# Optimization experiments

Hardware: AMD Instinct MI355X
Metric: run time of the kernel (lower is better)

The kernel has to match this reference:

```python
import jax, jax.numpy as jnp
import numpy as np

B, N_PER = 8, 16
N_ROIS = B * N_PER
C_SLOW, T_SLOW = 1024, 8
C_FAST, T_FAST = 256, 32
HF, WF = 16, 16
C_CAT = 2048          # channels after slow/fast concat
C_OUT = 1024          # 2048 // temporal_pool_size
T_POOL = 2
C_FEAT = C_OUT * T_POOL  # 2048 channels of the rearranged 2D feature map
OUT_SIZE = 16         # RoIAlign output size
RATIO = 2             # sampling_ratio
SCALE = 1.0 / 16.0    # 1 / featmap_stride
GN_GROUPS = 16
EPS = 1e-5


def setup_inputs() -> dict:
    key = jax.random.key(0)
    ks = jax.random.split(key, 8)
    slow_feat = jax.random.normal(ks[0], (B, C_SLOW, T_SLOW, HF, WF), jnp.float32)
    fast_feat = jax.random.normal(ks[1], (B, C_FAST, T_FAST, HF, WF), jnp.float32)
    pos = jax.random.normal(ks[2], (1, C_FEAT, HF, WF), jnp.float32)
    conv_w = jax.random.normal(ks[3], (C_OUT, C_CAT), jnp.float32) / np.float32(np.sqrt(C_CAT))
    gn_gamma = jnp.ones((C_OUT,), jnp.float32)
    gn_beta = jnp.zeros((C_OUT,), jnp.float32)
    # rois: [N,5] = (batch_idx, x1, y1, x2, y2) in input-image coords (256px clip).
    # Equal count per clip and sorted by batch idx -> grouping is a static reshape.
    bidx = jnp.repeat(jnp.arange(B), N_PER).astype(jnp.float32)
    cx = jax.random.uniform(ks[4], (N_ROIS,), minval=32.0, maxval=224.0)
    cy = jax.random.uniform(ks[5], (N_ROIS,), minval=32.0, maxval=224.0)
    w = jax.random.uniform(ks[6], (N_ROIS,), minval=32.0, maxval=160.0)
    h = jax.random.uniform(ks[7], (N_ROIS,), minval=32.0, maxval=160.0)
    x1 = jnp.clip(cx - w / 2, 0.0, 255.0)
    x2 = jnp.clip(cx + w / 2, 0.0, 255.0)
    y1 = jnp.clip(cy - h / 2, 0.0, 255.0)
    y2 = jnp.clip(cy + h / 2, 0.0, 255.0)
    rois = jnp.stack([bidx, x1, y1, x2, y2], axis=1)
    return dict(slow_feat=slow_feat, fast_feat=fast_feat, rois=rois, pos=pos,
                conv_w=conv_w, gn_gamma=gn_gamma, gn_beta=gn_beta)


def trans_feat(slow_feat, fast_feat, conv_w, gn_gamma, gn_beta):
    Bb, Cf, Tf, Wf_, Hf_ = fast_feat.shape
    ratio = 32 // slow_feat.shape[2]  # int(32 / T_slow)
    # fast: [B,C,T,W,H] -> [B,W,H,T,C] -> [B,W,H,T//r, C*r] -> [B, C*r, T//r, W, H]
    f = jnp.transpose(fast_feat, (0, 3, 4, 2, 1)).reshape(Bb, Wf_, Hf_, Tf // ratio, Cf * ratio)
    f = jnp.transpose(f, (0, 4, 3, 1, 2))
    feat = jnp.concatenate([slow_feat, f], axis=1)  # [B, 2048, T_slow, W, H]
    Bc, Cc, Tc, Wc, Hc = feat.shape
    # AdaptiveAvgPool3d((T_POOL, None, None)), Tc divisible by T_POOL
    feat = feat.reshape(Bc, Cc, T_POOL, Tc // T_POOL, Wc, Hc).mean(axis=3)
    # 1x1x1 Conv3d (no bias) -> GroupNorm(16) -> ReLU
    y = jnp.einsum('oc,bcthw->bothw', conv_w, feat)
    yg = y.reshape(Bc, GN_GROUPS, C_OUT // GN_GROUPS, T_POOL, Wc, Hc)
    mu = yg.mean(axis=(2, 3, 4, 5), keepdims=True)
    var = ((yg - mu) ** 2).mean(axis=(2, 3, 4, 5), keepdims=True)
    yg = (yg - mu) * jax.lax.rsqrt(var + EPS)
    y = yg.reshape(Bc, C_OUT, T_POOL, Wc, Hc)
    y = y * gn_gamma[None, :, None, None, None] + gn_beta[None, :, None, None, None]
    y = jax.nn.relu(y)
    # rearrange 'b c t w h -> b (c t) w h'
    return y.reshape(Bc, C_OUT * T_POOL, Wc, Hc)


def roialign_weights(rois):
    # mmcv RoIAlign (aligned=True, avg pool, sampling_ratio=RATIO) as a sparse
    # linear map over flattened feature pixels: out[n,:,p] = Wmat[n,p,:] @ feat[n,:,:]
    x1 = rois[:, 1] * SCALE - 0.5
    y1 = rois[:, 2] * SCALE - 0.5
    x2 = rois[:, 3] * SCALE - 0.5
    y2 = rois[:, 4] * SCALE - 0.5
    bw = (x2 - x1) / OUT_SIZE
    bh = (y2 - y1) / OUT_SIZE
    grid = (jnp.arange(OUT_SIZE, dtype=jnp.float32)[:, None]
            + (jnp.arange(RATIO, dtype=jnp.float32)[None, :] + 0.5) / RATIO)  # [O, r]
    ys = y1[:, None, None] + grid[None] * bh[:, None, None]  # [N, O, r]
    xs = x1[:, None, None] + grid[None] * bw[:, None, None]
    Y = jnp.broadcast_to(ys[:, :, None, :, None], (N_ROIS, OUT_SIZE, OUT_SIZE, RATIO, RATIO))
    X = jnp.broadcast_to(xs[:, None, :, None, :], (N_ROIS, OUT_SIZE, OUT_SIZE, RATIO, RATIO))
    valid = ((Y >= -1.0) & (Y <= HF) & (X >= -1.0) & (X <= WF)).astype(jnp.float32)
    y = jnp.maximum(Y, 0.0)
    x = jnp.maximum(X, 0.0)
    y0f = jnp.floor(y)
    x0f = jnp.floor(x)
    ye = y0f >= HF - 1
    xe = x0f >= WF - 1
    y0 = jnp.where(ye, HF - 1, y0f).astype(jnp.int32)
    y1i = jnp.where(ye, HF - 1, y0f + 1).astype(jnp.int32)
    x0 = jnp.where(xe, WF - 1, x0f).astype(jnp.int32)
    x1i = jnp.where(xe, WF - 1, x0f + 1).astype(jnp.int32)
    ly = jnp.where(ye, 0.0, y - y0f)
    lx = jnp.where(xe, 0.0, x - x0f)
    hy = 1.0 - ly
    hx = 1.0 - lx
    cnt = float(RATIO * RATIO)
    w = jnp.stack([hy * hx, hy * lx, ly * hx, ly * lx], axis=-1) * (valid / cnt)[..., None]
    idx = jnp.stack([y0 * WF + x0, y0 * WF + x1i, y1i * WF + x0, y1i * WF + x1i], axis=-1)
    P = OUT_SIZE * OUT_SIZE
    K = RATIO * RATIO * 4
    idx = idx.reshape(N_ROIS, P, K)
    w = w.reshape(N_ROIS, P, K)
    Wmat = jnp.zeros((N_ROIS, P, HF * WF), jnp.float32)
    Wmat = Wmat.at[jnp.arange(N_ROIS)[:, None, None],
                   jnp.arange(P)[None, :, None], idx].add(w)
    return Wmat


def reference(slow_feat, fast_feat, rois, pos, conv_w, gn_gamma, gn_beta):
    feat = trans_feat(slow_feat, fast_feat, conv_w, gn_gamma, gn_beta)  # [B, 2048, 16, 16]
    Wmat = roialign_weights(rois)                 # [N, 256, 256]
    bidx = rois[:, 0].astype(jnp.int32)
    featN = feat[bidx].reshape(N_ROIS, C_FEAT, HF * WF)  # per-roi feature gather
    # RoIAlign -> AdaptiveAvgPool2d((1,1)) -> view(1, C)
    roi_feat = jnp.einsum('npq,ncq->ncp', Wmat, featN).mean(axis=-1)  # [N, 2048]
    posF = pos.reshape(C_FEAT, HF * WF)           # pos.repeat(B,...) is identical per clip
    roi_pos = jnp.einsum('npq,cq->ncp', Wmat, posF).mean(axis=-1)     # [N, 2048]
    # bucketing by batch idx; rois are sorted with N_PER per clip -> static reshape
    roi_feat_grouped = roi_feat.reshape(B, N_PER, C_FEAT)
    roi_pos_grouped = roi_pos.reshape(B, N_PER, C_FEAT)
    return feat, roi_feat_grouped, roi_pos_grouped
```

## Files before the change

kernel.cpp:

```cpp
#include <hip/hip_runtime.h>
#include <hip/hip_bf16.h>

#define WH 256
#define FEATSZ 4194304
#define ROISZ  262144

typedef short s16x4 __attribute__((ext_vector_type(4)));
typedef short s16x8 __attribute__((ext_vector_type(8)));
typedef float f32x4 __attribute__((ext_vector_type(4)));

__device__ inline void gld_lds16(void* lds, const void* g) {
  __builtin_amdgcn_global_load_lds(
      (const __attribute__((address_space(1))) unsigned int*)g,
      (__attribute__((address_space(3))) unsigned int*)lds,
      16, 0, 0);
}

__device__ inline unsigned short bf16u(float v) {
  __hip_bfloat16 h = __float2bfloat16(v);
  return *(unsigned short*)&h;
}

__device__ inline f32x4 ntload4(const float* p) {
  return __builtin_nontemporal_load((const f32x4*)p);
}

__global__ __launch_bounds__(256) void fused_pre_kernel(
    const float* __restrict__ slow, const float* __restrict__ fast,
    const float* __restrict__ conv_w, const float* __restrict__ rois,
    __hip_bfloat16* __restrict__ FpT, __hip_bfloat16* __restrict__ Wb,
    float* __restrict__ wbar)
{
  __shared__ unsigned short tile[64][258];
  int blk = blockIdx.x;
  int tid = threadIdx.x;

  if (blk < 512) {
    int g = blk & 31;
    int t = (blk >> 5) & 1;
    int b = blk >> 6;
    int w = tid >> 6, lane = tid & 63;
    int wh4 = lane * 4;

    if (g < 16) {
      #pragma unroll 4
      for (int i = 0; i < 16; ++i) {
        int ch_l = i * 4 + w;
        int c = g * 64 + ch_l;
        const float* p = slow + ((size_t)((b * 1024 + c) * 8 + 4 * t)) * WH + wh4;
        f32x4 v0 = ntload4(p);
        f32x4 v1 = ntload4(p + WH);
        f32x4 v2 = ntload4(p + 2 * WH);
        f32x4 v3 = ntload4(p + 3 * WH);
        s16x4 o;
        o[0] = (short)bf16u(0.25f * (v0.x + v1.x + v2.x + v3.x));
        o[1] = (short)bf16u(0.25f * (v0.y + v1.y + v2.y + v3.y));
        o[2] = (short)bf16u(0.25f * (v0.z + v1.z + v2.z + v3.z));
        o[3] = (short)bf16u(0.25f * (v0.w + v1.w + v2.w + v3.w));
        *(s16x4*)&tile[ch_l][wh4] = o;
      }
    } else {
      int hi = (g - 16) >> 2;
      int cfb = ((g - 16) & 3) * 64;
      #pragma unroll 4
      for (int i = 0; i < 16; ++i) {
        int ch_l = i * 4 + w;
        int cf = cfb + ch_l;
        const float* p = fast + ((size_t)((b * 256 + cf) * 32 + 16 * t + hi)) * WH + wh4;
        f32x4 v0 = ntload4(p);
        f32x4 v1 = ntload4(p + 4 * WH);
        f32x4 v2 = ntload4(p + 8 * WH);
        f32x4 v3 = ntload4(p + 12 * WH);
        s16x4 o;
        o[0] = (short)bf16u(0.25f * (v0.x + v1.x + v2.x + v3.x));
        o[1] = (short)bf16u(0.25f * (v0.y + v1.y + v2.y + v3.y));
        o[2] = (short)bf16u(0.25f * (v0.z + v1.z + v2.z + v3.z));
        o[3] = (short)bf16u(0.25f * (v0.w + v1.w + v2.w + v3.w));
        *(s16x4*)&tile[ch_l][wh4] = o;
      }
    }
    __syncthreads();

    int c0 = (lane & 7) * 8;
    int col0 = (b * 2 + t) * 256;
    #pragma unroll
    for (int p = 0; p < 8; ++p) {
      int col_l = p * 32 + w * 8 + (lane >> 3);
      s16x8 o;
      #pragma unroll
      for (int j = 0; j < 8; ++j)
        o[j] = (short)tile[c0 + j][col_l];
      *(s16x8*)((char*)FpT + (size_t)(col0 + col_l) * 4096 + g * 128 + (lane & 7) * 16) = o;
    }
  } else if (blk < 576) {
    int tg = (blk - 512) * 256 + tid;
    #pragma unroll 4
    for (int j = 0; j < 32; ++j) {
      int idx = (j * 16384 + tg) * 4;
      f32x4 v = ntload4(conv_w + idx);
      s16x4 o;
      o[0] = (short)bf16u(v.x);
      o[1] = (short)bf16u(v.y);
      o[2] = (short)bf16u(v.z);
      o[3] = (short)bf16u(v.w);
      *(s16x4*)(Wb + idx) = o;
    }
  } else {
    float* acc = (float*)tile;
    int n = blk - 576;
    acc[tid] = 0.f;
    __syncthreads();
    const float* r = rois + n * 5;
    float x1 = r[1] * (1.f / 16.f) - 0.5f;
    float y1 = r[2] * (1.f / 16.f) - 0.5f;
    float x2 = r[3] * (1.f / 16.f) - 0.5f;
    float y2 = r[4] * (1.f / 16.f) - 0.5f;
    float bw = (x2 - x1) / 16.f;
    float bh = (y2 - y1) / 16.f;
    int py = tid >> 4, px = tid & 15;
    #pragma unroll
    for (int sy = 0; sy < 2; ++sy) {
      #pragma unroll
      for (int sx = 0; sx < 2; ++sx) {
        float gy = (float)py + (sy + 0.5f) * 0.5f;
        float gx = (float)px + (sx + 0.5f) * 0.5f;
        float Yv = y1 + gy * bh;
        float Xv = x1 + gx * bw;
        if (Yv >= -1.f && Yv <= 16.f && Xv >= -1.f && Xv <= 16.f) {
          float y = fmaxf(Yv, 0.f);
          float x = fmaxf(Xv, 0.f);
          float y0f = floorf(y);
          float x0f = floorf(x);
          bool ye = y0f >= 15.f;
          bool xe = x0f >= 15.f;
          int y0 = ye ? 15 : (int)y0f;
          int y1i = ye ? 15 : y0 + 1;
          int x0 = xe ? 15 : (int)x0f;
          int x1i = xe ? 15 : x0 + 1;
          float ly = ye ? 0.f : (y - y0f);
          float lx = xe ? 0.f : (x - x0f);
          float hy = 1.f - ly, hx = 1.f - lx;
          atomicAdd(&acc[y0 * 16 + x0], hy * hx);
          atomicAdd(&acc[y0 * 16 + x1i], hy * lx);
          atomicAdd(&acc[y1i * 16 + x0], ly * hx);
          atomicAdd(&acc[y1i * 16 + x1i], ly * lx);
        }
      }
    }
    __syncthreads();
    wbar[n * 256 + tid] = acc[tid] * (1.f / 1024.f);
  }
}

__global__ __launch_bounds__(256) void gemm_kernel(
    const __hip_bfloat16* __restrict__ Wb,
    const __hip_bfloat16* __restrict__ FpT,
    __hip_bfloat16* __restrict__ Yb,
    float2* __restrict__ partials)
{
  __shared__ unsigned short lA[128 * 64];
  __shared__ unsigned short lB[64 * 64];
  const int tid = threadIdx.x;
  const int lane = tid & 63;
  const int wid = tid >> 6;
  const int wm = wid >> 1, wn = wid & 1;
  const int nb = blockIdx.x, mb = blockIdx.y;
  const int lr8 = lane >> 3;
  const int lk  = lane & 7;

  f32x4 acc[4][2] = {};

  for (int k0 = 0; k0 < 2048; k0 += 64) {
    __syncthreads();
    #pragma unroll
    for (int j = 0; j < 4; ++j) {
      int row = wid * 32 + j * 8 + lr8;
      int kslot = lk ^ (row & 7);
      const __hip_bfloat16* g = Wb + (size_t)(mb * 128 + row) * 2048 + k0 + kslot * 8;
      gld_lds16(&lA[(wid * 32 + j * 8) * 64], g);
    }
    #pragma unroll
    for (int j = 0; j < 2; ++j) {
      int row = wid * 16 + j * 8 + lr8;
      int kslot = lk ^ (row & 7);
      const __hip_bfloat16* g = FpT + (size_t)(nb * 64 + row) * 2048 + k0 + kslot * 8;
      gld_lds16(&lB[(wid * 16 + j * 8) * 64], g);
    }
    __syncthreads();

    #pragma unroll
    for (int s = 0; s < 2; ++s) {
      s16x8 af[4], bf[2];
      #pragma unroll
      for (int mi = 0; mi < 4; ++mi) {
        int row = wm * 64 + mi * 16 + (lane & 15);
        int kslot = (s * 4 + (lane >> 4)) ^ (row & 7);
        af[mi] = *(const s16x8*)((const char*)lA + (row << 7) + (kslot << 4));
      }
      #pragma unroll
      for (int ni = 0; ni < 2; ++ni) {
        int row = wn * 32 + ni * 16 + (lane & 15);
        int kslot = (s * 4 + (lane >> 4)) ^ (row & 7);
        bf[ni] = *(const s16x8*)((const char*)lB + (row << 7) + (kslot << 4));
      }
      #pragma unroll
      for (int mi = 0; mi < 4; ++mi)
        #pragma unroll
        for (int ni = 0; ni < 2; ++ni)
          acc[mi][ni] = __builtin_amdgcn_mfma_f32_16x16x32_bf16(af[mi], bf[ni], acc[mi][ni], 0, 0, 0);
    }
  }

  float s = 0.f, ss = 0.f;
  #pragma unroll
  for (int mi = 0; mi < 4; ++mi) {
    #pragma unroll
    for (int ni = 0; ni < 2; ++ni) {
      int col = nb * 64 + wn * 32 + ni * 16 + (lane & 15);
      int o0 = mb * 128 + wm * 64 + mi * 16 + (lane >> 4) * 4;
      #pragma unroll
      for (int r = 0; r < 4; ++r) {
        float v = acc[mi][ni][r];
        Yb[(size_t)(o0 + r) * 4096 + col] = __float2bfloat16(v);
        s += v;
        ss += v * v;
      }
    }
  }
  #pragma unroll
  for (int off = 32; off; off >>= 1) {
    s += __shfl_xor(s, off);
    ss += __shfl_xor(ss, off);
  }
  if (lane == 0) {
    int b = nb >> 3;
    int g = 2 * mb + wm;
    partials[(b * 16 + g) * 16 + (nb & 7) * 2 + wn] = make_float2(s, ss);
  }
}

__global__ __launch_bounds__(256) void gn_kernel(
    const __hip_bfloat16* __restrict__ Yb, const float2* __restrict__ partials,
    const float* __restrict__ gamma, const float* __restrict__ beta,
    float* __restrict__ out)
{
  int blk = blockIdx.x;
  int q = blk & 15;
  int bg = blk >> 4;
  int b = bg >> 4, g = bg & 15;
  const float2* pp = partials + bg * 16;
  float S = 0.f, SS = 0.f;
  #pragma unroll
  for (int j = 0; j < 16; ++j) { float2 v = pp[j]; S += v.x; SS += v.y; }
  float mu = S * (1.f / 32768.f);
  float var = SS * (1.f / 32768.f) - mu * mu;
  float rstd = rsqrtf(var + 1e-5f);

  int tid = threadIdx.x;
  int o_l = q * 4 + (tid >> 6);
  int o = g * 64 + o_l;
  int colpos = (tid & 63) * 8;
  const __hip_bfloat16* src = Yb + (size_t)o * 4096 + b * 512 + colpos;
  float ga = gamma[o] * rstd, be = beta[o] - mu * rstd * gamma[o];
  int t = colpos >> 8, wh = colpos & 255;
  float* dst = out + ((size_t)(b * 2048 + o * 2 + t)) * 256 + wh;
  s16x8 yv = *(const s16x8*)src;
  #pragma unroll
  for (int j = 0; j < 2; ++j) {
    float4 r;
    r.x = fmaxf(__uint_as_float((unsigned)(unsigned short)yv[j * 4 + 0] << 16) * ga + be, 0.f);
    r.y = fmaxf(__uint_as_float((unsigned)(unsigned short)yv[j * 4 + 1] << 16) * ga + be, 0.f);
    r.z = fmaxf(__uint_as_float((unsigned)(unsigned short)yv[j * 4 + 2] << 16) * ga + be, 0.f);
    r.w = fmaxf(__uint_as_float((unsigned)(unsigned short)yv[j * 4 + 3] << 16) * ga + be, 0.f);
    *(float4*)(dst + j * 4) = r;
  }
}

__global__ __launch_bounds__(256) void roi_kernel(
    const float* __restrict__ feat, const float* __restrict__ pos,
    const float* __restrict__ wbar, float* __restrict__ out)
{
  __shared__ float wl[16][256];
  __shared__ float sF[2][16][128];
  __shared__ float sP[2][16][128];
  int b = blockIdx.x >> 4;
  int chunk = blockIdx.x & 15;
  int tid = threadIdx.x;
  #pragma unroll
  for (int rr = 0; rr < 16; ++rr)
    wl[rr][tid] = wbar[(b * 16 + rr) * 256 + tid];
  __syncthreads();
  int ch_l = tid & 127;
  int half = tid >> 7;
  int ch = chunk * 128 + ch_l;
  const float* fb = feat + ((size_t)(b * 2048 + ch)) * 256 + half * 128;
  const float* pb = pos + (size_t)ch * 256 + half * 128;
  float accF[16] = {0.f}, accP[16] = {0.f};
  for (int q0 = 0; q0 < 128; q0 += 4) {
    float4 vf = *(const float4*)(fb + q0);
    float4 vp = *(const float4*)(pb + q0);
    int q = half * 128 + q0;
    #pragma unroll
    for (int rr = 0; rr < 16; ++rr) {
      float4 w = *(const float4*)&wl[rr][q];
      accF[rr] += w.x * vf.x + w.y * vf.y + w.z * vf.z + w.w * vf.w;
      accP[rr] += w.x * vp.x + w.y * vp.y + w.z * vp.z + w.w * vp.w;
    }
  }
  #pragma unroll
  for (int rr = 0; rr < 16; ++rr) {
    sF[half][rr][ch_l] = accF[rr];
    sP[half][rr][ch_l] = accP[rr];
  }
  __syncthreads();
  if (half == 0) {
    #pragma unroll
    for (int rr = 0; rr < 16; ++rr) {
      float vF = sF[0][rr][ch_l] + sF[1][rr][ch_l];
      float vP = sP[0][rr][ch_l] + sP[1][rr][ch_l];
      out[FEATSZ + (size_t)(b * 16 + rr) * 2048 + ch] = vF;
      out[FEATSZ + ROISZ + (size_t)(b * 16 + rr) * 2048 + ch] = vP;
    }
  }
}

extern "C" void kernel_launch(void* const* d_in, const int* in_sizes, int n_in,
                              void* d_out, int out_size, void* d_ws, size_t ws_size,
                              hipStream_t stream)
{
  (void)in_sizes; (void)n_in; (void)out_size; (void)ws_size;
  const float* slow   = (const float*)d_in[0];
  const float* fast   = (const float*)d_in[1];
  const float* rois   = (const float*)d_in[2];
  const float* pos    = (const float*)d_in[3];
  const float* conv_w = (const float*)d_in[4];
  const float* gamma  = (const float*)d_in[5];
  const float* beta   = (const float*)d_in[6];
  float* out = (float*)d_out;
  char* ws = (char*)d_ws;

  __hip_bfloat16* FpT = (__hip_bfloat16*)(ws);
  __hip_bfloat16* Yb  = (__hip_bfloat16*)(ws + (16u << 20));
  __hip_bfloat16* Wb  = (__hip_bfloat16*)(ws + (24u << 20));
  float* wbar         = (float*)(ws + (28u << 20));
  float2* partials    = (float2*)(ws + (28u << 20) + (128u << 10));

  fused_pre_kernel<<<dim3(704), dim3(256), 0, stream>>>(
      slow, fast, conv_w, rois, FpT, Wb, wbar);
  gemm_kernel<<<dim3(64, 8), dim3(256), 0, stream>>>(Wb, FpT, Yb, partials);
  gn_kernel<<<dim3(2048), dim3(256), 0, stream>>>(Yb, partials, gamma, beta, out);
  roi_kernel<<<dim3(128), dim3(256), 0, stream>>>(out, pos, wbar, out);
}
```

Before: 86.68 us.

## Fuse GroupNorm and RoI pooling into one kernel; drop nontemporal loads

Merges the GroupNorm/ReLU kernel with the RoI-average kernel. Each thread now takes its 8 normalized values straight from registers, dots them against the per-RoI spatial weights held in LDS, and reduces with wave shuffles. This removes re-reading the 16 MB feature output and one kernel launch. The cost is that every block reloads 16 KB of weights into LDS and runs 16 shuffle reductions. Separately, nontemporal loads in the preprocessing kernel are replaced with plain loads.

New measurement: 77.60 us. -10.5%, faster.

```diff
diff --git a/kernel.cpp b/kernel.cpp
--- a/kernel.cpp
+++ b/kernel.cpp
@@ -21,9 +21,7 @@
   return *(unsigned short*)&h;
 }
 
-__device__ inline f32x4 ntload4(const float* p) {
-  return __builtin_nontemporal_load((const f32x4*)p);
-}
+__device__ inline f32x4 ld4(const float* p) { return *(const f32x4*)p; }
 
 __global__ __launch_bounds__(256) void fused_pre_kernel(
     const float* __restrict__ slow, const float* __restrict__ fast,
@@ -48,10 +46,10 @@
         int ch_l = i * 4 + w;
         int c = g * 64 + ch_l;
         const float* p = slow + ((size_t)((b * 1024 + c) * 8 + 4 * t)) * WH + wh4;
-        f32x4 v0 = ntload4(p);
-        f32x4 v1 = ntload4(p + WH);
-        f32x4 v2 = ntload4(p + 2 * WH);
-        f32x4 v3 = ntload4(p + 3 * WH);
+        f32x4 v0 = ld4(p);
+        f32x4 v1 = ld4(p + WH);
+        f32x4 v2 = ld4(p + 2 * WH);
+        f32x4 v3 = ld4(p + 3 * WH);
         s16x4 o;
         o[0] = (short)bf16u(0.25f * (v0.x + v1.x + v2.x + v3.x));
         o[1] = (short)bf16u(0.25f * (v0.y + v1.y + v2.y + v3.y));
@@ -67,10 +65,10 @@
         int ch_l = i * 4 + w;
         int cf = cfb + ch_l;
         const float* p = fast + ((size_t)((b * 256 + cf) * 32 + 16 * t + hi)) * WH + wh4;
-        f32x4 v0 = ntload4(p);
-        f32x4 v1 = ntload4(p + 4 * WH);
-        f32x4 v2 = ntload4(p + 8 * WH);
-        f32x4 v3 = ntload4(p + 12 * WH);
+        f32x4 v0 = ld4(p);
+        f32x4 v1 = ld4(p + 4 * WH);
+        f32x4 v2 = ld4(p + 8 * WH);
+        f32x4 v3 = ld4(p + 12 * WH);
         s16x4 o;
         o[0] = (short)bf16u(0.25f * (v0.x + v1.x + v2.x + v3.x));
         o[1] = (short)bf16u(0.25f * (v0.y + v1.y + v2.y + v3.y));
@@ -97,7 +95,7 @@
     #pragma unroll 4
     for (int j = 0; j < 32; ++j) {
       int idx = (j * 16384 + tg) * 4;
-      f32x4 v = ntload4(conv_w + idx);
+      f32x4 v = ld4(conv_w + idx);
       s16x4 o;
       o[0] = (short)bf16u(v.x);
       o[1] = (short)bf16u(v.y);
@@ -239,15 +237,23 @@
   }
 }
 
-__global__ __launch_bounds__(256) void gn_kernel(
+__global__ __launch_bounds__(256) void gn_roi_kernel(
     const __hip_bfloat16* __restrict__ Yb, const float2* __restrict__ partials,
     const float* __restrict__ gamma, const float* __restrict__ beta,
+    const float* __restrict__ pos, const float* __restrict__ wbar,
     float* __restrict__ out)
 {
+  __shared__ float wl[16][256];
   int blk = blockIdx.x;
   int q = blk & 15;
   int bg = blk >> 4;
   int b = bg >> 4, g = bg & 15;
+  int tid = threadIdx.x;
+  #pragma unroll
+  for (int n = 0; n < 16; ++n)
+    wl[n][tid] = wbar[(b * 16 + n) * 256 + tid];
+  __syncthreads();
+
   const float2* pp = partials + bg * 16;
   float S = 0.f, SS = 0.f;
   #pragma unroll
@@ -256,70 +262,44 @@
   float var = SS * (1.f / 32768.f) - mu * mu;
   float rstd = rsqrtf(var + 1e-5f);
 
-  int tid = threadIdx.x;
   int o_l = q * 4 + (tid >> 6);
   int o = g * 64 + o_l;
-  int colpos = (tid & 63) * 8;
-  const __hip_bfloat16* src = Yb + (size_t)o * 4096 + b * 512 + colpos;
+  int lane = tid & 63;
+  int colpos = lane * 8;
+  int t = colpos >> 8;
+  int wh0 = colpos & 255;
+  int c = o * 2 + t;
   float ga = gamma[o] * rstd, be = beta[o] - mu * rstd * gamma[o];
-  int t = colpos >> 8, wh = colpos & 255;
-  float* dst = out + ((size_t)(b * 2048 + o * 2 + t)) * 256 + wh;
-  s16x8 yv = *(const s16x8*)src;
-  #pragma unroll
-  for (int j = 0; j < 2; ++j) {
-    float4 r;
-    r.x = fmaxf(__uint_as_float((unsigned)(unsigned short)yv[j * 4 + 0] << 16) * ga + be, 0.f);
-    r.y = fmaxf(__uint_as_float((unsigned)(unsigned short)yv[j * 4 + 1] << 16) * ga + be, 0.f);
-    r.z = fmaxf(__uint_as_float((unsigned)(unsigned short)yv[j * 4 + 2] << 16) * ga + be, 0.f);
-    r.w = fmaxf(__uint_as_float((unsigned)(unsigned short)yv[j * 4 + 3] << 16) * ga + be, 0.f);
-    *(float4*)(dst + j * 4) = r;
-  }
-}
-
-__global__ __launch_bounds__(256) void roi_kernel(
-    const float* __restrict__ feat, const float* __restrict__ pos,
-    const float* __restrict__ wbar, float* __restrict__ out)
-{
-  __shared__ float wl[16][256];
-  __shared__ float sF[2][16][128];
-  __shared__ float sP[2][16][128];
-  int b = blockIdx.x >> 4;
-  int chunk = blockIdx.x & 15;
-  int tid = threadIdx.x;
-  #pragma unroll
-  for (int rr = 0; rr < 16; ++rr)
-    wl[rr][tid] = wbar[(b * 16 + rr) * 256 + tid];
-  __syncthreads();
-  int ch_l = tid & 127;
-  int half = tid >> 7;
-  int ch = chunk * 128 + ch_l;
-  const float* fb = feat + ((size_t)(b * 2048 + ch)) * 256 + half * 128;
-  const float* pb = pos + (size_t)ch * 256 + half * 128;
-  float accF[16] = {0.f}, accP[16] = {0.f};
-  for (int q0 = 0; q0 < 128; q0 += 4) {
-    float4 vf = *(const float4*)(fb + q0);
-    float4 vp = *(const float4*)(pb + q0);
-    int q = half * 128 + q0;
-    #pragma unroll
-    for (int rr = 0; rr < 16; ++rr) {
-      float4 w = *(const float4*)&wl[rr][q];
-      accF[rr] += w.x * vf.x + w.y * vf.y + w.z * vf.z + w.w * vf.w;
-      accP[rr] += w.x * vp.x + w.y * vp.y + w.z * vp.z + w.w * vp.w;
-    }
-  }
-  #pragma unroll
-  for (int rr = 0; rr < 16; ++rr) {
-    sF[half][rr][ch_l] = accF[rr];
-    sP[half][rr][ch_l] = accP[rr];
-  }
-  __syncthreads();
-  if (half == 0) {
-    #pragma unroll
-    for (int rr = 0; rr < 16; ++rr) {
-      float vF = sF[0][rr][ch_l] + sF[1][rr][ch_l];
-      float vP = sP[0][rr][ch_l] + sP[1][rr][ch_l];
-      out[FEATSZ + (size_t)(b * 16 + rr) * 2048 + ch] = vF;
-      out[FEATSZ + ROISZ + (size_t)(b * 16 + rr) * 2048 + ch] = vP;
+
+  s16x8 yv = *(const s16x8*)(Yb + (size_t)o * 4096 + b * 512 + colpos);
+  float f[8];
+  #pragma unroll
+  for (int j = 0; j < 8; ++j)
+    f[j] = fmaxf(__uint_as_float((unsigned)(unsigned short)yv[j] << 16) * ga + be, 0.f);
+
+  float* dst = out + ((size_t)(b * 2048 + c)) * 256 + wh0;
+  *(float4*)dst = make_float4(f[0], f[1], f[2], f[3]);
+  *(float4*)(dst + 4) = make_float4(f[4], f[5], f[6], f[7]);
+
+  float4 p0 = *(const float4*)(pos + (size_t)c * 256 + wh0);
+  float4 p1 = *(const float4*)(pos + (size_t)c * 256 + wh0 + 4);
+
+  #pragma unroll
+  for (int n = 0; n < 16; ++n) {
+    float4 w0 = *(const float4*)&wl[n][wh0];
+    float4 w1 = *(const float4*)&wl[n][wh0 + 4];
+    float aF = w0.x * f[0] + w0.y * f[1] + w0.z * f[2] + w0.w * f[3]
+             + w1.x * f[4] + w1.y * f[5] + w1.z * f[6] + w1.w * f[7];
+    float aP = w0.x * p0.x + w0.y * p0.y + w0.z * p0.z + w0.w * p0.w
+             + w1.x * p1.x + w1.y * p1.y + w1.z * p1.z + w1.w * p1.w;
+    #pragma unroll
+    for (int off = 1; off < 32; off <<= 1) {
+      aF += __shfl_xor(aF, off, 32);
+      aP += __shfl_xor(aP, off, 32);
+    }
+    if ((lane & 31) == 0) {
+      out[FEATSZ + (size_t)(b * 16 + n) * 2048 + c] = aF;
+      out[FEATSZ + ROISZ + (size_t)(b * 16 + n) * 2048 + c] = aP;
     }
   }
 }
@@ -348,6 +328,6 @@
   fused_pre_kernel<<<dim3(704), dim3(256), 0, stream>>>(
       slow, fast, conv_w, rois, FpT, Wb, wbar);
   gemm_kernel<<<dim3(64, 8), dim3(256), 0, stream>>>(Wb, FpT, Yb, partials);
-  gn_kernel<<<dim3(2048), dim3(256), 0, stream>>>(Yb, partials, gamma, beta, out);
-  roi_kernel<<<dim3(128), dim3(256), 0, stream>>>(out, pos, wbar, out);
-}
+  gn_roi_kernel<<<dim3(2048), dim3(256), 0, stream>>>(
+      Yb, partials, gamma, beta, pos, wbar, out);
+}
```
